# Performance work log

Hardware: AMD Instinct MI355X
Metric: run time of the kernel (lower is better)

## Reference

```python
import jax, jax.numpy as jnp
import numpy as np

N_NODES = 163840
N_EDGES = 2621440
F_IN = 64
F_HID = 64
SUBG = 20  # size_subgraph_samples
NEG_SLOPE = 0.2


def gat_conv(x, src, dst, W, a_src, a_dst, b):
    """PyG GATConv, heads=1, concat. src/dst already include self-loops."""
    n = x.shape[0]
    h = x @ W                               # [N, H]
    al_s = h @ a_src                        # [N]
    al_d = h @ a_dst                        # [N]
    e = jax.nn.leaky_relu(al_s[src] + al_d[dst], NEG_SLOPE)  # [E]
    # softmax over incoming edges of each dst node
    m = jax.ops.segment_max(e, dst, num_segments=n)
    ex = jnp.exp(e - m[dst])
    denom = jax.ops.segment_sum(ex, dst, num_segments=n)
    alpha = ex / (denom[dst] + 1e-16)
    msg = h[src] * alpha[:, None]           # [E, H]
    out = jax.ops.segment_sum(msg, dst, num_segments=n)
    return out + b


def setup_inputs() -> dict:
    key = jax.random.key(0)
    ks = jax.random.split(key, 12)
    s = 0.05
    return {
        "x": jax.random.normal(ks[0], (N_NODES, F_IN), jnp.float32),
        "edge_index": jax.random.randint(ks[1], (2, N_EDGES), 0, N_NODES, jnp.int64 if jax.config.jax_enable_x64 else jnp.int32),
        "W1": jax.random.normal(ks[2], (F_IN, F_HID), jnp.float32) * s,
        "a_src1": jax.random.normal(ks[3], (F_HID,), jnp.float32) * s,
        "a_dst1": jax.random.normal(ks[4], (F_HID,), jnp.float32) * s,
        "b1": jnp.zeros((F_HID,), jnp.float32),
        "W2": jax.random.normal(ks[5], (F_HID, F_HID), jnp.float32) * s,
        "a_src2": jax.random.normal(ks[6], (F_HID,), jnp.float32) * s,
        "a_dst2": jax.random.normal(ks[7], (F_HID,), jnp.float32) * s,
        "b2": jnp.zeros((F_HID,), jnp.float32),
        "W_out": jax.random.normal(ks[8], (F_HID * SUBG, 1), jnp.float32) * s,
        "b_out": jnp.zeros((1,), jnp.float32),
    }


def reference(x, edge_index, W1, a_src1, a_dst1, b1, W2, a_src2, a_dst2, b2, W_out, b_out):
    n = x.shape[0]
    loop = jnp.arange(n, dtype=edge_index.dtype)
    src = jnp.concatenate([edge_index[0], loop])  # add_self_loops=True
    dst = jnp.concatenate([edge_index[1], loop])
    h = gat_conv(x, src, dst, W1, a_src1, a_dst1, b1)
    h = jax.nn.relu(h)  # dropout is identity in eval mode
    h = gat_conv(h, src, dst, W2, a_src2, a_dst2, b2)
    h = jax.nn.relu(h)
    h = h.reshape(n // SUBG, F_HID * SUBG)
    return h @ W_out + b_out
```

## Files before the change

### kernel.cpp

```cpp
#include <hip/hip_runtime.h>
#include <math.h>

#define F 64
#define NPB 160
#define STAGE_CAP 6304
#define BCAP 3584

typedef __attribute__((ext_vector_type(8))) short bf16x8;
typedef __attribute__((ext_vector_type(4))) float f32x4;

__device__ inline unsigned short f2bf(float f) {
  unsigned int u = __float_as_uint(f);
  u += 0x7fffu + ((u >> 16) & 1u);
  return (unsigned short)(u >> 16);
}

__global__ __launch_bounds__(256) void k_prep(const float* __restrict__ W1, const float* __restrict__ W2,
                                              uint4* __restrict__ wf, int* __restrict__ bcnt, int nb,
                                              float* __restrict__ out, const float* __restrict__ bo, int ng) {
  int tid = threadIdx.x;
  if (blockIdx.x == 0) {
    for (int i = tid; i < 1024; i += 256) {
      int layer = i >> 9, rem = i & 511;
      int cb = rem >> 6, lane = rem & 63;
      int c = cb >> 1, kk = cb & 1;
      int l15 = lane & 15, quad = lane >> 4;
      const float* W = layer ? W2 : W1;
      unsigned short p[8];
      #pragma unroll
      for (int j = 0; j < 8; j++) {
        int kd = kk * 32 + quad * 8 + j;
        p[j] = f2bf(W[kd * F + c * 16 + l15]);
      }
      wf[i] = *(const uint4*)p;
    }
  } else {
    for (int i = tid; i < nb * 16; i += 256) bcnt[i] = 0;
    float b0 = bo[0];
    for (int i = tid; i < ng; i += 256) out[i] = b0;
  }
}

template<bool IN_BF16>
__device__ __forceinline__ void gemm_body(const void* __restrict__ in, const uint4* __restrict__ wf,
                                          const float* __restrict__ avs, const float* __restrict__ avd,
                                          unsigned short* __restrict__ hgb, float* __restrict__ als,
                                          float* __restrict__ ald, int n, int bid, int nbl) {
  int tid = threadIdx.x, lane = tid & 63, wv = tid >> 6;
  int l15 = lane & 15, quad = lane >> 4;
  bf16x8 bfr[4][2];
  #pragma unroll
  for (int cb = 0; cb < 8; cb++) {
    uint4 u = wf[cb * 64 + lane];
    bfr[cb >> 1][cb & 1] = *(const bf16x8*)&u;
  }
  float as_l[4], ad_l[4];
  #pragma unroll
  for (int c = 0; c < 4; c++) { as_l[c] = avs[c * 16 + l15]; ad_l[c] = avd[c * 16 + l15]; }

  int nchunks = n >> 6;
  for (int chunk = bid; chunk < nchunks; chunk += nbl) {
    int r0 = (chunk << 6) + (wv << 4);
    bf16x8 a0, a1;
    if constexpr (IN_BF16) {
      const uint4* row4 = (const uint4*)((const unsigned short*)in + (size_t)(r0 + l15) * F);
      uint4 u0 = row4[quad];
      uint4 u1 = row4[quad + 4];
      a0 = *(const bf16x8*)&u0;
      a1 = *(const bf16x8*)&u1;
    } else {
      const float4* xr = (const float4*)((const float*)in + (size_t)(r0 + l15) * F + quad * 8);
      float4 xa = xr[0], xb = xr[1];
      float4 xc = xr[8], xd = xr[9];
      a0[0] = (short)f2bf(xa.x); a0[1] = (short)f2bf(xa.y); a0[2] = (short)f2bf(xa.z); a0[3] = (short)f2bf(xa.w);
      a0[4] = (short)f2bf(xb.x); a0[5] = (short)f2bf(xb.y); a0[6] = (short)f2bf(xb.z); a0[7] = (short)f2bf(xb.w);
      a1[0] = (short)f2bf(xc.x); a1[1] = (short)f2bf(xc.y); a1[2] = (short)f2bf(xc.z); a1[3] = (short)f2bf(xc.w);
      a1[4] = (short)f2bf(xd.x); a1[5] = (short)f2bf(xd.y); a1[6] = (short)f2bf(xd.z); a1[7] = (short)f2bf(xd.w);
    }
    f32x4 cfr[4];
    #pragma unroll
    for (int c = 0; c < 4; c++) {
      cfr[c] = (f32x4){0.f, 0.f, 0.f, 0.f};
      cfr[c] = __builtin_amdgcn_mfma_f32_16x16x32_bf16(a0, bfr[c][0], cfr[c], 0, 0, 0);
      cfr[c] = __builtin_amdgcn_mfma_f32_16x16x32_bf16(a1, bfr[c][1], cfr[c], 0, 0, 0);
    }
    #pragma unroll
    for (int i = 0; i < 4; i++) {
      int row = r0 + quad * 4 + i;
      #pragma unroll
      for (int c = 0; c < 4; c++) hgb[(size_t)row * F + c * 16 + l15] = f2bf(cfr[c][i]);
      float ps = cfr[0][i] * as_l[0] + cfr[1][i] * as_l[1] + cfr[2][i] * as_l[2] + cfr[3][i] * as_l[3];
      float pd = cfr[0][i] * ad_l[0] + cfr[1][i] * ad_l[1] + cfr[2][i] * ad_l[2] + cfr[3][i] * ad_l[3];
      #pragma unroll
      for (int o = 1; o <= 8; o <<= 1) { ps += __shfl_xor(ps, o); pd += __shfl_xor(pd, o); }
      if (l15 == 0) { als[row] = ps; ald[row] = pd; }
    }
  }
}

__global__ __launch_bounds__(256) void k_scatter_gemm1(const int* __restrict__ esrc, const int* __restrict__ edst,
                                                       int* __restrict__ bcnt, unsigned int* __restrict__ binned,
                                                       int e, int ch, int S,
                                                       const float* __restrict__ x, const uint4* __restrict__ wf,
                                                       const float* __restrict__ avs, const float* __restrict__ avd,
                                                       unsigned short* __restrict__ hgb, float* __restrict__ als,
                                                       float* __restrict__ ald, int n) {
  int k = blockIdx.x, tid = threadIdx.x;
  if (k < S) {
    __shared__ int hist[1024];
    __shared__ int cur[1024];
    for (int i = tid; i < 1024; i += 256) hist[i] = 0;
    __syncthreads();
    int beg = k * ch, end = min(e, beg + ch);
    int len = end - beg;
    if (len <= 0) return;
    int nv = len >> 2;
    for (int g = tid; g < nv; g += 256) {
      int4 d4 = *(const int4*)(edst + beg + (g << 2));
      atomicAdd(&hist[d4.x / NPB], 1);
      atomicAdd(&hist[d4.y / NPB], 1);
      atomicAdd(&hist[d4.z / NPB], 1);
      atomicAdd(&hist[d4.w / NPB], 1);
    }
    for (int i = beg + (nv << 2) + tid; i < end; i += 256) atomicAdd(&hist[edst[i] / NPB], 1);
    __syncthreads();
    for (int b = tid; b < 1024; b += 256) {
      int c = hist[b];
      int base = 0;
      if (c) base = atomicAdd(&bcnt[b * 16], c);
      cur[b] = b * BCAP + base;
    }
    __syncthreads();
    for (int g = tid; g < nv; g += 256) {
      int i = beg + (g << 2);
      int4 d4 = *(const int4*)(edst + i);
      int4 s4 = *(const int4*)(esrc + i);
      #pragma unroll
      for (int j = 0; j < 4; j++) {
        int d = (j == 0) ? d4.x : (j == 1) ? d4.y : (j == 2) ? d4.z : d4.w;
        int s = (j == 0) ? s4.x : (j == 1) ? s4.y : (j == 2) ? s4.z : s4.w;
        int b = d / NPB;
        int p = atomicAdd(&cur[b], 1);
        if (p < (b + 1) * BCAP) binned[p] = (unsigned int)s | ((unsigned int)(d - b * NPB) << 24);
      }
    }
    for (int i = beg + (nv << 2) + tid; i < end; i += 256) {
      int d = edst[i];
      int b = d / NPB;
      int p = atomicAdd(&cur[b], 1);
      if (p < (b + 1) * BCAP) binned[p] = (unsigned int)esrc[i] | ((unsigned int)(d - b * NPB) << 24);
    }
    return;
  }
  gemm_body<false>(x, wf, avs, avd, hgb, als, ald, n, k - S, (int)gridDim.x - S);
}

__global__ __launch_bounds__(256) void k_bucket_scan(const int* __restrict__ bcnt, int* __restrict__ obase,
                                                     int* __restrict__ offs, int n, int nb) {
  __shared__ int wsum[4];
  __shared__ int carry_sh;
  int tid = threadIdx.x, lane = tid & 63, wv = tid >> 6;
  if (tid == 0) carry_sh = 0;
  __syncthreads();
  for (int base = 0; base < nb; base += 256) {
    int b = base + tid;
    int v = 0;
    if (b < nb) {
      int cnt = min(bcnt[b * 16], BCAP);
      int nn = min(NPB, n - b * NPB);
      v = cnt + nn;
    }
    int x = v;
    #pragma unroll
    for (int o = 1; o <= 32; o <<= 1) { int y = __shfl_up(x, o); if (lane >= o) x += y; }
    if (lane == 63) wsum[wv] = x;
    __syncthreads();
    int add = 0;
    for (int w = 0; w < wv; w++) add += wsum[w];
    int incl = x + add;
    int carry = carry_sh;
    if (b < nb) obase[b] = incl - v + carry;
    __syncthreads();
    if (tid == 255) carry_sh = carry + incl;
    __syncthreads();
  }
  if (tid == 0) offs[n] = carry_sh;
}

__global__ __launch_bounds__(256) void k_bucket_csr(const unsigned int* __restrict__ binned,
                                                    const int* __restrict__ bcnt, const int* __restrict__ obase,
                                                    int* __restrict__ ssrc, int* __restrict__ offs, int n) {
  __shared__ int ncnt[NPB];
  __shared__ int noff[NPB];
  __shared__ int cur[NPB];
  __shared__ int sc[256];
  __shared__ int stage[STAGE_CAP];
  int b = blockIdx.x, tid = threadIdx.x;
  int node0 = b * NPB;
  int nn = min(NPB, n - node0);
  int ebeg = b * BCAP;
  int ecnt = min(bcnt[b * 16], BCAP);
  int outbase = obase[b];
  for (int i = tid; i < NPB; i += 256) ncnt[i] = 0;
  __syncthreads();
  for (int i = tid; i < ecnt; i += 256) { unsigned int v = binned[ebeg + i]; atomicAdd(&ncnt[v >> 24], 1); }
  __syncthreads();
  int x = (tid < nn) ? ncnt[tid] + 1 : 0;
  sc[tid] = x;
  __syncthreads();
  #pragma unroll
  for (int o = 1; o < 256; o <<= 1) {
    int y = (tid >= o) ? sc[tid - o] : 0;
    __syncthreads();
    sc[tid] += y;
    __syncthreads();
  }
  if (tid < nn) noff[tid] = sc[tid] - x;
  __syncthreads();
  int tot = ecnt + nn;
  bool staged = (tot <= STAGE_CAP);
  if (tid < nn) {
    cur[tid] = noff[tid] + 1;
    offs[node0 + tid] = outbase + noff[tid];
    if (staged) stage[noff[tid]] = node0 + tid;
    else        ssrc[outbase + noff[tid]] = node0 + tid;
  }
  __syncthreads();
  if (staged) {
    for (int i = tid; i < ecnt; i += 256) {
      unsigned int v = binned[ebeg + i];
      int p = atomicAdd(&cur[v >> 24], 1);
      stage[p] = (int)(v & 0xFFFFFFu);
    }
    __syncthreads();
    for (int i = tid; i < tot; i += 256) ssrc[outbase + i] = stage[i];
  } else {
    for (int i = tid; i < ecnt; i += 256) {
      unsigned int v = binned[ebeg + i];
      int p = atomicAdd(&cur[v >> 24], 1);
      ssrc[outbase + p] = (int)(v & 0xFFFFFFu);
    }
  }
}

__global__ __launch_bounds__(256) void k_gemm2(const unsigned short* __restrict__ in, const uint4* __restrict__ wf,
                                               const float* __restrict__ avs, const float* __restrict__ avd,
                                               unsigned short* __restrict__ hgb, float* __restrict__ als,
                                               float* __restrict__ ald, int n) {
  gemm_body<true>(in, wf, avs, avd, hgb, als, ald, n, blockIdx.x, gridDim.x);
}

template<int MODE>
__global__ __launch_bounds__(256) void k_spmm(const int* __restrict__ offs, const int* __restrict__ ssrc,
                                              const unsigned short* __restrict__ hgb,
                                              const float* __restrict__ als, const float* __restrict__ ald,
                                              const float* __restrict__ bias, const float* __restrict__ Wout,
                                              void* __restrict__ outp, int n) {
  int tid = threadIdx.x, lane = tid & 63, wv = tid >> 6;
  int g8 = lane >> 3, l8 = lane & 7;
  const uint4* hg4 = (const uint4*)hgb;
  float4 bl0 = ((const float4*)bias)[l8 * 2];
  float4 bl1 = ((const float4*)bias)[l8 * 2 + 1];

  __shared__ float gsl[3];
  if (MODE == 1 && tid < 3) gsl[tid] = 0.f;

  int node = (blockIdx.x * 4 + wv) * 8 + g8;
  int cnode = min(node, n - 1);
  bool nodeok = node < n;
  int beg = offs[cnode];
  int deg = nodeok ? (offs[cnode + 1] - beg) : 0;
  int degc = max(deg - 1, 0);
  float aldv = ald[cnode];

  int dm = deg;
  #pragma unroll
  for (int o = 8; o <= 32; o <<= 1) dm = max(dm, __shfl_xor(dm, o));

  float s = 0.f;
  float acc[8];
  #pragma unroll
  for (int k = 0; k < 8; k++) acc[k] = 0.f;

  #pragma unroll 2
  for (int j = 0; j < dm; j++) {
    int jj = min(j, degc);
    int src = ssrc[beg + jj];
    float t = als[src] + aldv;
    t = fmaxf(t, 0.2f * t);
    float ex = (j < deg) ? __expf(t) : 0.f;
    s += ex;
    uint4 u = hg4[(size_t)src * 8 + l8];
    acc[0] = fmaf(ex, __uint_as_float(u.x << 16), acc[0]);
    acc[1] = fmaf(ex, __uint_as_float(u.x & 0xffff0000u), acc[1]);
    acc[2] = fmaf(ex, __uint_as_float(u.y << 16), acc[2]);
    acc[3] = fmaf(ex, __uint_as_float(u.y & 0xffff0000u), acc[3]);
    acc[4] = fmaf(ex, __uint_as_float(u.z << 16), acc[4]);
    acc[5] = fmaf(ex, __uint_as_float(u.z & 0xffff0000u), acc[5]);
    acc[6] = fmaf(ex, __uint_as_float(u.w << 16), acc[6]);
    acc[7] = fmaf(ex, __uint_as_float(u.w & 0xffff0000u), acc[7]);
  }

  float iv = 1.f / (s + 1e-16f);
  float r[8];
  r[0] = fmaxf(fmaf(acc[0], iv, bl0.x), 0.f);
  r[1] = fmaxf(fmaf(acc[1], iv, bl0.y), 0.f);
  r[2] = fmaxf(fmaf(acc[2], iv, bl0.z), 0.f);
  r[3] = fmaxf(fmaf(acc[3], iv, bl0.w), 0.f);
  r[4] = fmaxf(fmaf(acc[4], iv, bl1.x), 0.f);
  r[5] = fmaxf(fmaf(acc[5], iv, bl1.y), 0.f);
  r[6] = fmaxf(fmaf(acc[6], iv, bl1.z), 0.f);
  r[7] = fmaxf(fmaf(acc[7], iv, bl1.w), 0.f);

  if constexpr (MODE == 0) {
    if (!nodeok) return;
    unsigned short p[8];
    #pragma unroll
    for (int k = 0; k < 8; k++) p[k] = f2bf(r[k]);
    ((uint4*)outp)[(size_t)node * 8 + l8] = *(const uint4*)p;
  } else {
    int node0 = blockIdx.x * 32;
    int grp0 = node0 / 20;
    int grp = cnode / 20, slot = cnode - grp * 20;
    const float* wr = Wout + slot * F + l8 * 8;
    float dot = 0.f;
    #pragma unroll
    for (int k = 0; k < 8; k++) dot = fmaf(r[k], wr[k], dot);
    #pragma unroll
    for (int o = 1; o <= 4; o <<= 1) dot += __shfl_xor(dot, o);
    __syncthreads();
    if (nodeok && l8 == 0) atomicAdd(&gsl[grp - grp0], dot);
    __syncthreads();
    if (tid < 3) {
      float v = gsl[tid];
      if (v != 0.f) atomicAdd((float*)outp + grp0 + tid, v);
    }
  }
}

extern "C" void kernel_launch(void* const* d_in, const int* in_sizes, int n_in,
                              void* d_out, int out_size, void* d_ws, size_t ws_size,
                              hipStream_t stream) {
  const float* x   = (const float*)d_in[0];
  const int*   ei  = (const int*)d_in[1];
  const float* W1  = (const float*)d_in[2];
  const float* as1 = (const float*)d_in[3];
  const float* ad1 = (const float*)d_in[4];
  const float* b1  = (const float*)d_in[5];
  const float* W2  = (const float*)d_in[6];
  const float* as2 = (const float*)d_in[7];
  const float* ad2 = (const float*)d_in[8];
  const float* b2  = (const float*)d_in[9];
  const float* Wo  = (const float*)d_in[10];
  const float* bo  = (const float*)d_in[11];
  float* out = (float*)d_out;

  const int N = in_sizes[0] / F;
  const int E = in_sizes[1] / 2;
  const int* esrc = ei;
  const int* edst = ei + E;

  size_t off = 0;
  auto alloc = [&](size_t bytes) -> void* {
    void* p = (char*)d_ws + off;
    off += (bytes + 255) & ~(size_t)255;
    return p;
  };
  float* A    = (float*)alloc((size_t)N * F * 4);
  unsigned short* hgb = (unsigned short*)alloc((size_t)N * F * 2);
  float* als  = (float*)alloc((size_t)N * 4);
  float* ald  = (float*)alloc((size_t)N * 4);
  int* offs   = (int*)alloc((size_t)(N + 1) * 4);
  int* bcnt   = (int*)alloc((size_t)1024 * 16 * 4);
  int* obase  = (int*)alloc((size_t)1024 * 4);
  int* ssrc   = (int*)alloc((size_t)(E + N) * 4);
  uint4* wf   = (uint4*)alloc(16384);
  (void)ws_size; (void)n_in; (void)out_size;

  const int S = 256;
  const int NB = (N + NPB - 1) / NPB;
  const int CH = (((E + S - 1) / S) + 3) & ~3;
  const int NG = N / 20;

  unsigned int* binned = (unsigned int*)((char*)A + (size_t)8 * 1024 * 1024);

  k_prep<<<2, 256, 0, stream>>>(W1, W2, wf, bcnt, NB, out, bo, NG);
  k_scatter_gemm1<<<S + (N >> 6), 256, 0, stream>>>(esrc, edst, bcnt, binned, E, CH, S,
                                                    x, wf, as1, ad1, hgb, als, ald, N);
  k_bucket_scan<<<1, 256, 0, stream>>>(bcnt, obase, offs, N, NB);
  k_bucket_csr<<<NB, 256, 0, stream>>>(binned, bcnt, obase, ssrc, offs, N);

  int gSp = (N + 31) / 32;
  k_spmm<0><<<gSp, 256, 0, stream>>>(offs, ssrc, hgb, als, ald, b1, nullptr, A, N);
  k_gemm2<<<(N >> 6), 256, 0, stream>>>((const unsigned short*)A, wf + 512, as2, ad2, hgb, als, ald, N);
  k_spmm<1><<<gSp, 256, 0, stream>>>(offs, ssrc, hgb, als, ald, b2, Wo, out, N);
}
```

Measured before the change: 295.0 us.

## Replace bucketed CSR build with per-node counting sort and fuse layer-1 aggregation with GEMM2

Drops the two-level bucket binning and local CSR build. It now counts per-node in-degrees with global atomics, runs a two-kernel scan, and scatters sources straight into CSR with per-node atomic cursors. Self-loops are handled inline in the aggregation instead of being stored in the CSR. Layer-1 aggregation is fused with the layer-2 GEMM through shared memory, so the fp32 intermediate buffer is never written or re-read. The cost is heavy global atomic contention on 2.6M edges, random scattered writes, and more kernel launches for the scan.

```diff
diff --git a/kernel.cpp b/kernel.cpp
--- a/kernel.cpp
+++ b/kernel.cpp
@@ -2,9 +2,6 @@
 #include <math.h>
 
 #define F 64
-#define NPB 160
-#define STAGE_CAP 6304
-#define BCAP 3584
 
 typedef __attribute__((ext_vector_type(8))) short bf16x8;
 typedef __attribute__((ext_vector_type(4))) float f32x4;
@@ -16,7 +13,7 @@
 }
 
 __global__ __launch_bounds__(256) void k_prep(const float* __restrict__ W1, const float* __restrict__ W2,
-                                              uint4* __restrict__ wf, int* __restrict__ bcnt, int nb,
+                                              uint4* __restrict__ wf, int* __restrict__ ndeg, int n,
                                               float* __restrict__ out, const float* __restrict__ bo, int ng) {
   int tid = threadIdx.x;
   if (blockIdx.x == 0) {
@@ -35,14 +32,73 @@
       wf[i] = *(const uint4*)p;
     }
   } else {
-    for (int i = tid; i < nb * 16; i += 256) bcnt[i] = 0;
+    int base = (blockIdx.x - 1) * 256 + tid;
+    int stride = 255 * 256;
+    for (int i = base; i < n; i += stride) ndeg[i] = 0;
     float b0 = bo[0];
-    for (int i = tid; i < ng; i += 256) out[i] = b0;
-  }
-}
-
-template<bool IN_BF16>
-__device__ __forceinline__ void gemm_body(const void* __restrict__ in, const uint4* __restrict__ wf,
+    for (int i = base; i < ng; i += stride) out[i] = b0;
+  }
+}
+
+__global__ __launch_bounds__(256) void k_count(const int* __restrict__ edst, int* __restrict__ ndeg,
+                                               int e, int ch) {
+  int k = blockIdx.x, tid = threadIdx.x;
+  int beg = k * ch, end = min(e, beg + ch);
+  int len = end - beg;
+  if (len <= 0) return;
+  int nv = len >> 2;
+  for (int g = tid; g < nv; g += 256) {
+    int4 d4 = *(const int4*)(edst + beg + (g << 2));
+    atomicAdd(&ndeg[d4.x], 1);
+    atomicAdd(&ndeg[d4.y], 1);
+    atomicAdd(&ndeg[d4.z], 1);
+    atomicAdd(&ndeg[d4.w], 1);
+  }
+  for (int i = beg + (nv << 2) + tid; i < end; i += 256) atomicAdd(&ndeg[edst[i]], 1);
+}
+
+__global__ __launch_bounds__(256) void k_scan1(const int* __restrict__ counts, int* __restrict__ ppos,
+                                               int* __restrict__ bsums, int n) {
+  int tid = threadIdx.x, lane = tid & 63, wv = tid >> 6;
+  int i = blockIdx.x * 256 + tid;
+  int v = (i < n) ? counts[i] : 0;
+  int x = v;
+  #pragma unroll
+  for (int o = 1; o <= 32; o <<= 1) { int y = __shfl_up(x, o); if (lane >= o) x += y; }
+  __shared__ int wsum[4];
+  if (lane == 63) wsum[wv] = x;
+  __syncthreads();
+  int add = 0;
+  for (int w = 0; w < wv; w++) add += wsum[w];
+  int incl = x + add;
+  if (i < n) ppos[i] = incl - v;
+  if (tid == 255) bsums[blockIdx.x] = incl;
+}
+
+__global__ __launch_bounds__(256) void k_init(const int* __restrict__ ppos, const int* __restrict__ bsums,
+                                              int* __restrict__ offs, int* __restrict__ cur,
+                                              int* __restrict__ ssrc, int n, int e) {
+  __shared__ int rbuf[256];
+  int tid = threadIdx.x, b = blockIdx.x;
+  int acc = 0;
+  for (int t = tid; t < b; t += 256) acc += bsums[t];
+  rbuf[tid] = acc;
+  __syncthreads();
+  #pragma unroll
+  for (int o = 128; o > 0; o >>= 1) {
+    if (tid < o) rbuf[tid] += rbuf[tid + o];
+    __syncthreads();
+  }
+  int sb = rbuf[0];
+  int i = b * 256 + tid;
+  if (i < n) { int o = ppos[i] + sb; offs[i] = o; cur[i] = o; }
+  if (b == 0) {
+    if (tid == 0) offs[n] = e;
+    if (tid < 16) ssrc[e + tid] = 0;
+  }
+}
+
+__device__ __forceinline__ void gemm_body(const float* __restrict__ in, const uint4* __restrict__ wf,
                                           const float* __restrict__ avs, const float* __restrict__ avd,
                                           unsigned short* __restrict__ hgb, float* __restrict__ als,
                                           float* __restrict__ ald, int n, int bid, int nbl) {
@@ -62,21 +118,13 @@
   for (int chunk = bid; chunk < nchunks; chunk += nbl) {
     int r0 = (chunk << 6) + (wv << 4);
     bf16x8 a0, a1;
-    if constexpr (IN_BF16) {
-      const uint4* row4 = (const uint4*)((const unsigned short*)in + (size_t)(r0 + l15) * F);
-      uint4 u0 = row4[quad];
-      uint4 u1 = row4[quad + 4];
-      a0 = *(const bf16x8*)&u0;
-      a1 = *(const bf16x8*)&u1;
-    } else {
-      const float4* xr = (const float4*)((const float*)in + (size_t)(r0 + l15) * F + quad * 8);
-      float4 xa = xr[0], xb = xr[1];
-      float4 xc = xr[8], xd = xr[9];
-      a0[0] = (short)f2bf(xa.x); a0[1] = (short)f2bf(xa.y); a0[2] = (short)f2bf(xa.z); a0[3] = (short)f2bf(xa.w);
-      a0[4] = (short)f2bf(xb.x); a0[5] = (short)f2bf(xb.y); a0[6] = (short)f2bf(xb.z); a0[7] = (short)f2bf(xb.w);
-      a1[0] = (short)f2bf(xc.x); a1[1] = (short)f2bf(xc.y); a1[2] = (short)f2bf(xc.z); a1[3] = (short)f2bf(xc.w);
-      a1[4] = (short)f2bf(xd.x); a1[5] = (short)f2bf(xd.y); a1[6] = (short)f2bf(xd.z); a1[7] = (short)f2bf(xd.w);
-    }
+    const float4* xr = (const float4*)(in + (size_t)(r0 + l15) * F + quad * 8);
+    float4 xa = xr[0], xb = xr[1];
+    float4 xc = xr[8], xd = xr[9];
+    a0[0] = (short)f2bf(xa.x); a0[1] = (short)f2bf(xa.y); a0[2] = (short)f2bf(xa.z); a0[3] = (short)f2bf(xa.w);
+    a0[4] = (short)f2bf(xb.x); a0[5] = (short)f2bf(xb.y); a0[6] = (short)f2bf(xb.z); a0[7] = (short)f2bf(xb.w);
+    a1[0] = (short)f2bf(xc.x); a1[1] = (short)f2bf(xc.y); a1[2] = (short)f2bf(xc.z); a1[3] = (short)f2bf(xc.w);
+    a1[4] = (short)f2bf(xd.x); a1[5] = (short)f2bf(xd.y); a1[6] = (short)f2bf(xd.z); a1[7] = (short)f2bf(xd.w);
     f32x4 cfr[4];
     #pragma unroll
     for (int c = 0; c < 4; c++) {
@@ -99,7 +147,7 @@
 }
 
 __global__ __launch_bounds__(256) void k_scatter_gemm1(const int* __restrict__ esrc, const int* __restrict__ edst,
-                                                       int* __restrict__ bcnt, unsigned int* __restrict__ binned,
+                                                       int* __restrict__ cur, int* __restrict__ ssrc,
                                                        int e, int ch, int S,
                                                        const float* __restrict__ x, const uint4* __restrict__ wf,
                                                        const float* __restrict__ avs, const float* __restrict__ avd,
@@ -107,182 +155,61 @@
                                                        float* __restrict__ ald, int n) {
   int k = blockIdx.x, tid = threadIdx.x;
   if (k < S) {
-    __shared__ int hist[1024];
-    __shared__ int cur[1024];
-    for (int i = tid; i < 1024; i += 256) hist[i] = 0;
-    __syncthreads();
     int beg = k * ch, end = min(e, beg + ch);
     int len = end - beg;
     if (len <= 0) return;
     int nv = len >> 2;
     for (int g = tid; g < nv; g += 256) {
-      int4 d4 = *(const int4*)(edst + beg + (g << 2));
-      atomicAdd(&hist[d4.x / NPB], 1);
-      atomicAdd(&hist[d4.y / NPB], 1);
-      atomicAdd(&hist[d4.z / NPB], 1);
-      atomicAdd(&hist[d4.w / NPB], 1);
-    }
-    for (int i = beg + (nv << 2) + tid; i < end; i += 256) atomicAdd(&hist[edst[i] / NPB], 1);
-    __syncthreads();
-    for (int b = tid; b < 1024; b += 256) {
-      int c = hist[b];
-      int base = 0;
-      if (c) base = atomicAdd(&bcnt[b * 16], c);
-      cur[b] = b * BCAP + base;
-    }
-    __syncthreads();
-    for (int g = tid; g < nv; g += 256) {
       int i = beg + (g << 2);
       int4 d4 = *(const int4*)(edst + i);
       int4 s4 = *(const int4*)(esrc + i);
-      #pragma unroll
-      for (int j = 0; j < 4; j++) {
-        int d = (j == 0) ? d4.x : (j == 1) ? d4.y : (j == 2) ? d4.z : d4.w;
-        int s = (j == 0) ? s4.x : (j == 1) ? s4.y : (j == 2) ? s4.z : s4.w;
-        int b = d / NPB;
-        int p = atomicAdd(&cur[b], 1);
-        if (p < (b + 1) * BCAP) binned[p] = (unsigned int)s | ((unsigned int)(d - b * NPB) << 24);
-      }
+      int p0 = atomicAdd(&cur[d4.x], 1);
+      int p1 = atomicAdd(&cur[d4.y], 1);
+      int p2 = atomicAdd(&cur[d4.z], 1);
+      int p3 = atomicAdd(&cur[d4.w], 1);
+      ssrc[p0] = s4.x; ssrc[p1] = s4.y; ssrc[p2] = s4.z; ssrc[p3] = s4.w;
     }
     for (int i = beg + (nv << 2) + tid; i < end; i += 256) {
-      int d = edst[i];
-      int b = d / NPB;
-      int p = atomicAdd(&cur[b], 1);
-      if (p < (b + 1) * BCAP) binned[p] = (unsigned int)esrc[i] | ((unsigned int)(d - b * NPB) << 24);
+      int p = atomicAdd(&cur[edst[i]], 1);
+      ssrc[p] = esrc[i];
     }
     return;
   }
-  gemm_body<false>(x, wf, avs, avd, hgb, als, ald, n, k - S, (int)gridDim.x - S);
-}
-
-__global__ __launch_bounds__(256) void k_bucket_scan(const int* __restrict__ bcnt, int* __restrict__ obase,
-                                                     int* __restrict__ offs, int n, int nb) {
-  __shared__ int wsum[4];
-  __shared__ int carry_sh;
-  int tid = threadIdx.x, lane = tid & 63, wv = tid >> 6;
-  if (tid == 0) carry_sh = 0;
-  __syncthreads();
-  for (int base = 0; base < nb; base += 256) {
-    int b = base + tid;
-    int v = 0;
-    if (b < nb) {
-      int cnt = min(bcnt[b * 16], BCAP);
-      int nn = min(NPB, n - b * NPB);
-      v = cnt + nn;
-    }
-    int x = v;
-    #pragma unroll
-    for (int o = 1; o <= 32; o <<= 1) { int y = __shfl_up(x, o); if (lane >= o) x += y; }
-    if (lane == 63) wsum[wv] = x;
-    __syncthreads();
-    int add = 0;
-    for (int w = 0; w < wv; w++) add += wsum[w];
-    int incl = x + add;
-    int carry = carry_sh;
-    if (b < nb) obase[b] = incl - v + carry;
-    __syncthreads();
-    if (tid == 255) carry_sh = carry + incl;
-    __syncthreads();
-  }
-  if (tid == 0) offs[n] = carry_sh;
-}
-
-__global__ __launch_bounds__(256) void k_bucket_csr(const unsigned int* __restrict__ binned,
-                                                    const int* __restrict__ bcnt, const int* __restrict__ obase,
-                                                    int* __restrict__ ssrc, int* __restrict__ offs, int n) {
-  __shared__ int ncnt[NPB];
-  __shared__ int noff[NPB];
-  __shared__ int cur[NPB];
-  __shared__ int sc[256];
-  __shared__ int stage[STAGE_CAP];
-  int b = blockIdx.x, tid = threadIdx.x;
-  int node0 = b * NPB;
-  int nn = min(NPB, n - node0);
-  int ebeg = b * BCAP;
-  int ecnt = min(bcnt[b * 16], BCAP);
-  int outbase = obase[b];
-  for (int i = tid; i < NPB; i += 256) ncnt[i] = 0;
-  __syncthreads();
-  for (int i = tid; i < ecnt; i += 256) { unsigned int v = binned[ebeg + i]; atomicAdd(&ncnt[v >> 24], 1); }
-  __syncthreads();
-  int x = (tid < nn) ? ncnt[tid] + 1 : 0;
-  sc[tid] = x;
-  __syncthreads();
-  #pragma unroll
-  for (int o = 1; o < 256; o <<= 1) {
-    int y = (tid >= o) ? sc[tid - o] : 0;
-    __syncthreads();
-    sc[tid] += y;
-    __syncthreads();
-  }
-  if (tid < nn) noff[tid] = sc[tid] - x;
-  __syncthreads();
-  int tot = ecnt + nn;
-  bool staged = (tot <= STAGE_CAP);
-  if (tid < nn) {
-    cur[tid] = noff[tid] + 1;
-    offs[node0 + tid] = outbase + noff[tid];
-    if (staged) stage[noff[tid]] = node0 + tid;
-    else        ssrc[outbase + noff[tid]] = node0 + tid;
-  }
-  __syncthreads();
-  if (staged) {
-    for (int i = tid; i < ecnt; i += 256) {
-      unsigned int v = binned[ebeg + i];
-      int p = atomicAdd(&cur[v >> 24], 1);
-      stage[p] = (int)(v & 0xFFFFFFu);
-    }
-    __syncthreads();
-    for (int i = tid; i < tot; i += 256) ssrc[outbase + i] = stage[i];
-  } else {
-    for (int i = tid; i < ecnt; i += 256) {
-      unsigned int v = binned[ebeg + i];
-      int p = atomicAdd(&cur[v >> 24], 1);
-      ssrc[outbase + p] = (int)(v & 0xFFFFFFu);
-    }
-  }
-}
-
-__global__ __launch_bounds__(256) void k_gemm2(const unsigned short* __restrict__ in, const uint4* __restrict__ wf,
-                                               const float* __restrict__ avs, const float* __restrict__ avd,
-                                               unsigned short* __restrict__ hgb, float* __restrict__ als,
-                                               float* __restrict__ ald, int n) {
-  gemm_body<true>(in, wf, avs, avd, hgb, als, ald, n, blockIdx.x, gridDim.x);
-}
-
-template<int MODE>
-__global__ __launch_bounds__(256) void k_spmm(const int* __restrict__ offs, const int* __restrict__ ssrc,
-                                              const unsigned short* __restrict__ hgb,
-                                              const float* __restrict__ als, const float* __restrict__ ald,
-                                              const float* __restrict__ bias, const float* __restrict__ Wout,
-                                              void* __restrict__ outp, int n) {
-  int tid = threadIdx.x, lane = tid & 63, wv = tid >> 6;
-  int g8 = lane >> 3, l8 = lane & 7;
-  const uint4* hg4 = (const uint4*)hgb;
-  float4 bl0 = ((const float4*)bias)[l8 * 2];
-  float4 bl1 = ((const float4*)bias)[l8 * 2 + 1];
-
-  __shared__ float gsl[3];
-  if (MODE == 1 && tid < 3) gsl[tid] = 0.f;
-
-  int node = (blockIdx.x * 4 + wv) * 8 + g8;
+  gemm_body(x, wf, avs, avd, hgb, als, ald, n, k - S, (int)gridDim.x - S);
+}
+
+__device__ __forceinline__ void agg_node(int node, int n, const int* __restrict__ offs,
+                                         const int* __restrict__ ssrc,
+                                         const uint4* __restrict__ hg4,
+                                         const float* __restrict__ als,
+                                         const float* __restrict__ ald,
+                                         float4 bl0, float4 bl1, int l8, float r[8]) {
   int cnode = min(node, n - 1);
-  bool nodeok = node < n;
   int beg = offs[cnode];
-  int deg = nodeok ? (offs[cnode + 1] - beg) : 0;
+  int deg = offs[cnode + 1] - beg;
   int degc = max(deg - 1, 0);
   float aldv = ald[cnode];
 
+  float ts = als[cnode] + aldv;
+  ts = fmaxf(ts, 0.2f * ts);
+  float exs = __expf(ts);
+  float s = exs;
+  uint4 us = hg4[(size_t)cnode * 8 + l8];
+  float acc[8];
+  acc[0] = exs * __uint_as_float(us.x << 16);
+  acc[1] = exs * __uint_as_float(us.x & 0xffff0000u);
+  acc[2] = exs * __uint_as_float(us.y << 16);
+  acc[3] = exs * __uint_as_float(us.y & 0xffff0000u);
+  acc[4] = exs * __uint_as_float(us.z << 16);
+  acc[5] = exs * __uint_as_float(us.z & 0xffff0000u);
+  acc[6] = exs * __uint_as_float(us.w << 16);
+  acc[7] = exs * __uint_as_float(us.w & 0xffff0000u);
+
   int dm = deg;
   #pragma unroll
   for (int o = 8; o <= 32; o <<= 1) dm = max(dm, __shfl_xor(dm, o));
 
-  float s = 0.f;
-  float acc[8];
-  #pragma unroll
-  for (int k = 0; k < 8; k++) acc[k] = 0.f;
-
-  #pragma unroll 2
+  #pragma unroll 4
   for (int j = 0; j < dm; j++) {
     int jj = min(j, degc);
     int src = ssrc[beg + jj];
@@ -302,7 +229,6 @@
   }
 
   float iv = 1.f / (s + 1e-16f);
-  float r[8];
   r[0] = fmaxf(fmaf(acc[0], iv, bl0.x), 0.f);
   r[1] = fmaxf(fmaf(acc[1], iv, bl0.y), 0.f);
   r[2] = fmaxf(fmaf(acc[2], iv, bl0.z), 0.f);
@@ -311,30 +237,105 @@
   r[5] = fmaxf(fmaf(acc[5], iv, bl1.y), 0.f);
   r[6] = fmaxf(fmaf(acc[6], iv, bl1.z), 0.f);
   r[7] = fmaxf(fmaf(acc[7], iv, bl1.w), 0.f);
-
-  if constexpr (MODE == 0) {
-    if (!nodeok) return;
-    unsigned short p[8];
-    #pragma unroll
-    for (int k = 0; k < 8; k++) p[k] = f2bf(r[k]);
-    ((uint4*)outp)[(size_t)node * 8 + l8] = *(const uint4*)p;
-  } else {
-    int node0 = blockIdx.x * 32;
-    int grp0 = node0 / 20;
-    int grp = cnode / 20, slot = cnode - grp * 20;
-    const float* wr = Wout + slot * F + l8 * 8;
-    float dot = 0.f;
-    #pragma unroll
-    for (int k = 0; k < 8; k++) dot = fmaf(r[k], wr[k], dot);
-    #pragma unroll
-    for (int o = 1; o <= 4; o <<= 1) dot += __shfl_xor(dot, o);
-    __syncthreads();
-    if (nodeok && l8 == 0) atomicAdd(&gsl[grp - grp0], dot);
-    __syncthreads();
-    if (tid < 3) {
-      float v = gsl[tid];
-      if (v != 0.f) atomicAdd((float*)outp + grp0 + tid, v);
-    }
+}
+
+__global__ __launch_bounds__(256) void k_spmm_g2(const int* __restrict__ offs, const int* __restrict__ ssrc,
+                                                 const unsigned short* __restrict__ hgb,
+                                                 const float* __restrict__ als, const float* __restrict__ ald,
+                                                 const float* __restrict__ bias, const uint4* __restrict__ wf2,
+                                                 const float* __restrict__ avs, const float* __restrict__ avd,
+                                                 unsigned short* __restrict__ hgb2, float* __restrict__ als2,
+                                                 float* __restrict__ ald2, int n) {
+  __shared__ __align__(16) unsigned short hsh[64][72];
+  int tid = threadIdx.x, lane = tid & 63, wv = tid >> 6;
+  int g8 = lane >> 3, l8 = lane & 7;
+  const uint4* hg4 = (const uint4*)hgb;
+  float4 bl0 = ((const float4*)bias)[l8 * 2];
+  float4 bl1 = ((const float4*)bias)[l8 * 2 + 1];
+
+  for (int p = 0; p < 2; p++) {
+    int row = p * 32 + wv * 8 + g8;
+    int node = blockIdx.x * 64 + row;
+    float r[8];
+    agg_node(node, n, offs, ssrc, hg4, als, ald, bl0, bl1, l8, r);
+    unsigned short pk[8];
+    #pragma unroll
+    for (int k = 0; k < 8; k++) pk[k] = f2bf(r[k]);
+    *(uint4*)&hsh[row][l8 * 8] = *(const uint4*)pk;
+  }
+  __syncthreads();
+
+  int l15 = lane & 15, quad = lane >> 4;
+  bf16x8 bfr[4][2];
+  #pragma unroll
+  for (int cb = 0; cb < 8; cb++) {
+    uint4 u = wf2[cb * 64 + lane];
+    bfr[cb >> 1][cb & 1] = *(const bf16x8*)&u;
+  }
+  float as_l[4], ad_l[4];
+  #pragma unroll
+  for (int c = 0; c < 4; c++) { as_l[c] = avs[c * 16 + l15]; ad_l[c] = avd[c * 16 + l15]; }
+
+  int r0 = wv << 4;
+  uint4 u0 = *(const uint4*)&hsh[r0 + l15][quad * 8];
+  uint4 u1 = *(const uint4*)&hsh[r0 + l15][quad * 8 + 32];
+  bf16x8 a0 = *(const bf16x8*)&u0;
+  bf16x8 a1 = *(const bf16x8*)&u1;
+  f32x4 cfr[4];
+  #pragma unroll
+  for (int c = 0; c < 4; c++) {
+    cfr[c] = (f32x4){0.f, 0.f, 0.f, 0.f};
+    cfr[c] = __builtin_amdgcn_mfma_f32_16x16x32_bf16(a0, bfr[c][0], cfr[c], 0, 0, 0);
+    cfr[c] = __builtin_amdgcn_mfma_f32_16x16x32_bf16(a1, bfr[c][1], cfr[c], 0, 0, 0);
+  }
+  #pragma unroll
+  for (int i = 0; i < 4; i++) {
+    int row = blockIdx.x * 64 + r0 + quad * 4 + i;
+    #pragma unroll
+    for (int c = 0; c < 4; c++) hgb2[(size_t)row * F + c * 16 + l15] = f2bf(cfr[c][i]);
+    float ps = cfr[0][i] * as_l[0] + cfr[1][i] * as_l[1] + cfr[2][i] * as_l[2] + cfr[3][i] * as_l[3];
+    float pd = cfr[0][i] * ad_l[0] + cfr[1][i] * ad_l[1] + cfr[2][i] * ad_l[2] + cfr[3][i] * ad_l[3];
+    #pragma unroll
+    for (int o = 1; o <= 8; o <<= 1) { ps += __shfl_xor(ps, o); pd += __shfl_xor(pd, o); }
+    if (l15 == 0) { als2[row] = ps; ald2[row] = pd; }
+  }
+}
+
+__global__ __launch_bounds__(256) void k_spmm_out(const int* __restrict__ offs, const int* __restrict__ ssrc,
+                                                  const unsigned short* __restrict__ hgb,
+                                                  const float* __restrict__ als, const float* __restrict__ ald,
+                                                  const float* __restrict__ bias, const float* __restrict__ Wout,
+                                                  float* __restrict__ out, int n) {
+  int tid = threadIdx.x, lane = tid & 63, wv = tid >> 6;
+  int g8 = lane >> 3, l8 = lane & 7;
+  const uint4* hg4 = (const uint4*)hgb;
+  float4 bl0 = ((const float4*)bias)[l8 * 2];
+  float4 bl1 = ((const float4*)bias)[l8 * 2 + 1];
+
+  __shared__ float gsl[3];
+  if (tid < 3) gsl[tid] = 0.f;
+
+  int node = (blockIdx.x * 4 + wv) * 8 + g8;
+  bool nodeok = node < n;
+  int cnode = min(node, n - 1);
+  float r[8];
+  agg_node(node, n, offs, ssrc, hg4, als, ald, bl0, bl1, l8, r);
+
+  int node0 = blockIdx.x * 32;
+  int grp0 = node0 / 20;
+  int grp = cnode / 20, slot = cnode - grp * 20;
+  const float* wr = Wout + slot * F + l8 * 8;
+  float dot = 0.f;
+  #pragma unroll
+  for (int k = 0; k < 8; k++) dot = fmaf(r[k], wr[k], dot);
+  #pragma unroll
+  for (int o = 1; o <= 4; o <<= 1) dot += __shfl_xor(dot, o);
+  __syncthreads();
+  if (nodeok && l8 == 0) atomicAdd(&gsl[grp - grp0], dot);
+  __syncthreads();
+  if (tid < 3) {
+    float v = gsl[tid];
+    if (v != 0.f) atomicAdd(out + grp0 + tid, v);
   }
 }
 
@@ -366,32 +367,33 @@
     off += (bytes + 255) & ~(size_t)255;
     return p;
   };
-  float* A    = (float*)alloc((size_t)N * F * 4);
-  unsigned short* hgb = (unsigned short*)alloc((size_t)N * F * 2);
+  unsigned short* hgb  = (unsigned short*)alloc((size_t)N * F * 2);
+  unsigned short* hgb2 = (unsigned short*)alloc((size_t)N * F * 2);
   float* als  = (float*)alloc((size_t)N * 4);
   float* ald  = (float*)alloc((size_t)N * 4);
+  float* als2 = (float*)alloc((size_t)N * 4);
+  float* ald2 = (float*)alloc((size_t)N * 4);
+  int* ndeg   = (int*)alloc((size_t)N * 4);
+  int* ppos   = (int*)alloc((size_t)N * 4);
+  int* cur    = (int*)alloc((size_t)N * 4);
   int* offs   = (int*)alloc((size_t)(N + 1) * 4);
-  int* bcnt   = (int*)alloc((size_t)1024 * 16 * 4);
-  int* obase  = (int*)alloc((size_t)1024 * 4);
-  int* ssrc   = (int*)alloc((size_t)(E + N) * 4);
+  int* bsums  = (int*)alloc(4096);
+  int* ssrc   = (int*)alloc((size_t)(E + 64) * 4);
   uint4* wf   = (uint4*)alloc(16384);
   (void)ws_size; (void)n_in; (void)out_size;
 
-  const int S = 256;
-  const int NB = (N + NPB - 1) / NPB;
-  const int CH = (((E + S - 1) / S) + 3) & ~3;
   const int NG = N / 20;
-
-  unsigned int* binned = (unsigned int*)((char*)A + (size_t)8 * 1024 * 1024);
-
-  k_prep<<<2, 256, 0, stream>>>(W1, W2, wf, bcnt, NB, out, bo, NG);
-  k_scatter_gemm1<<<S + (N >> 6), 256, 0, stream>>>(esrc, edst, bcnt, binned, E, CH, S,
-                                                    x, wf, as1, ad1, hgb, als, ald, N);
-  k_bucket_scan<<<1, 256, 0, stream>>>(bcnt, obase, offs, N, NB);
-  k_bucket_csr<<<NB, 256, 0, stream>>>(binned, bcnt, obase, ssrc, offs, N);
-
-  int gSp = (N + 31) / 32;
-  k_spmm<0><<<gSp, 256, 0, stream>>>(offs, ssrc, hgb, als, ald, b1, nullptr, A, N);
-  k_gemm2<<<(N >> 6), 256, 0, stream>>>((const unsigned short*)A, wf + 512, as2, ad2, hgb, als, ald, N);
-  k_spmm<1><<<gSp, 256, 0, stream>>>(offs, ssrc, hgb, als, ald, b2, Wo, out, N);
-}
+  const int gScan = (N + 255) / 256;
+  const int SC = 1024;
+  const int CH = (((E + SC - 1) / SC) + 3) & ~3;
+
+  k_prep<<<256, 256, 0, stream>>>(W1, W2, wf, ndeg, N, out, bo, NG);
+  k_count<<<SC, 256, 0, stream>>>(edst, ndeg, E, CH);
+  k_scan1<<<gScan, 256, 0, stream>>>(ndeg, ppos, bsums, N);
+  k_init<<<gScan, 256, 0, stream>>>(ppos, bsums, offs, cur, ssrc, N, E);
+  k_scatter_gemm1<<<SC + (N >> 6), 256, 0, stream>>>(esrc, edst, cur, ssrc, E, CH, SC,
+                                                     x, wf, as1, ad1, hgb, als, ald, N);
+  k_spmm_g2<<<(N >> 6), 256, 0, stream>>>(offs, ssrc, hgb, als, ald, b1, wf + 512, as2, ad2,
+                                          hgb2, als2, ald2, N);
+  k_spmm_out<<<(N >> 5), 256, 0, stream>>>(offs, ssrc, hgb2, als2, ald2, b2, Wo, out, N);
+}
```

New measurement: 560.2 us. 89.9% more time.
